# Performance work log

Measured on AMD Instinct MI355X. Metric: run time of the kernel, lower is better.

## Reference

```python
import jax, jax.numpy as jnp
import numpy as np

EPS = 1e-5
B, C, H, W, MIP, CQ = 2, 256, 64, 64, 8, 32  # MIP = max(8, C//32); CQ = C//8


def _bn(x, p):
    # inference BatchNorm; p is [4, C] = (gamma, beta, running_mean, running_var)
    g, b, m, v = p[0], p[1], p[2], p[3]
    s = g / jnp.sqrt(v + EPS)
    return x * s[None, :, None, None] + (b - m * s)[None, :, None, None]


def _c1(x, w):  # 1x1 conv, w: [O, I]
    return jnp.einsum('bchw,oc->bohw', x, w)


def _c3(x, w):  # 3x3 conv, SAME padding, w: [O, I, 3, 3]
    return jax.lax.conv_general_dilated(x, w, (1, 1), 'SAME',
                                        dimension_numbers=('NCHW', 'OIHW', 'NCHW'))


def _cbs1(x, w, p):  # Conv(1x1)+BN+SiLU (YOLOv7 Conv block)
    return jax.nn.silu(_bn(_c1(x, w), p))


def _cbs3(x, w, p):  # Conv(3x3)+BN+SiLU
    return jax.nn.silu(_bn(_c3(x, w), p))


def _maxpool(x, k):  # MaxPool2d(kernel=k, stride=1, padding=k//2)
    p = k // 2
    return jax.lax.reduce_window(x, -jnp.inf, jax.lax.max,
                                 (1, 1, k, k), (1, 1, 1, 1),
                                 ((0, 0), (0, 0), (p, p), (p, p)))


def setup_inputs() -> dict:
    ks = iter(jax.random.split(jax.random.key(0), 64))

    def rn(shape, scale):
        return jax.random.normal(next(ks), shape, jnp.float32) * scale

    def w_(o, i, k=1):  # fan-in scaled conv weight
        sc = 1.0 / float(np.sqrt(i * k * k))
        return rn((o, i) if k == 1 else (o, i, k, k), sc)

    def bnp(c):  # gamma, beta, running_mean, running_var (var > 0)
        return jnp.stack([1.0 + rn((c,), 0.05), rn((c,), 0.05), rn((c,), 0.05),
                          0.5 + jax.random.uniform(next(ks), (c,), jnp.float32)])

    cm = C  # SPPCSPC hidden: int(2*C*0.5) = C
    return dict(
        x=rn((B, C, H, W), 1.0),
        ca_w1=w_(MIP, C), ca_b1=rn((MIP,), 0.05), ca_bn=bnp(MIP),
        ca_wh=w_(C, MIP), ca_bh=rn((C,), 0.05),
        ca_ww=w_(C, MIP), ca_bw=rn((C,), 0.05),
        s1_w=w_(cm, C), s1_bn=bnp(cm),
        s2_w=w_(cm, C), s2_bn=bnp(cm),
        s3_w=w_(cm, cm, 3), s3_bn=bnp(cm),
        s4_w=w_(cm, cm), s4_bn=bnp(cm),
        s5_w=w_(cm, 4 * cm), s5_bn=bnp(cm),
        s6_w=w_(cm, cm, 3), s6_bn=bnp(cm),
        s7_w=w_(C, 2 * cm), s7_bn=bnp(C),
        pq_w=w_(CQ, C), pq_b=rn((CQ,), 0.05),
        pk_w=w_(CQ, C), pk_b=rn((CQ,), 0.05),
        pv_w=w_(C, C), pv_b=rn((C,), 0.05),
        gamma_pa=rn((1,), 1.0), gamma_ca=rn((1,), 1.0),
    )


def reference(x, ca_w1, ca_b1, ca_bn, ca_wh, ca_bh, ca_ww, ca_bw,
              s1_w, s1_bn, s2_w, s2_bn, s3_w, s3_bn, s4_w, s4_bn,
              s5_w, s5_bn, s6_w, s6_bn, s7_w, s7_bn,
              pq_w, pq_b, pk_w, pk_b, pv_w, pv_b, gamma_pa, gamma_ca):
    b, c, h, w = x.shape
    # ---- CoordAtt ----
    xh = jnp.mean(x, axis=3, keepdims=True)                                 # b,c,h,1
    xw = jnp.transpose(jnp.mean(x, axis=2, keepdims=True), (0, 1, 3, 2))    # b,c,w,1
    y = jnp.concatenate([xh, xw], axis=2)                                   # b,c,h+w,1
    y = _bn(_c1(y, ca_w1) + ca_b1[None, :, None, None], ca_bn)
    y = y * jnp.clip(y + 3.0, 0.0, 6.0) / 6.0                               # h_swish
    a_h = jax.nn.sigmoid(_c1(y[:, :, :h], ca_wh) + ca_bh[None, :, None, None])
    a_w = jax.nn.sigmoid(_c1(jnp.transpose(y[:, :, h:], (0, 1, 3, 2)), ca_ww)
                         + ca_bw[None, :, None, None])
    r = x * a_w * a_h
    # ---- SPPCSPC ----
    x1 = _cbs1(_cbs3(_cbs1(r, s1_w, s1_bn), s3_w, s3_bn), s4_w, s4_bn)
    cat = jnp.concatenate([x1] + [_maxpool(x1, k) for k in (5, 9, 13)], axis=1)
    y1 = _cbs3(_cbs1(cat, s5_w, s5_bn), s6_w, s6_bn)
    y2 = _cbs1(r, s2_w, s2_bn)
    res = _cbs1(jnp.concatenate([y1, y2], axis=1), s7_w, s7_bn)
    # ---- PAM (spatial attention) ----
    n = h * w
    f = res.reshape(b, c, n)
    q = jnp.einsum('bcn,oc->bon', f, pq_w) + pq_b[None, :, None]            # b,c/8,n
    k = jnp.einsum('bcn,oc->bon', f, pk_w) + pk_b[None, :, None]
    v = jnp.einsum('bcn,oc->bon', f, pv_w) + pv_b[None, :, None]            # b,c,n
    attn = jax.nn.softmax(jnp.einsum('bcn,bcm->bnm', q, k), axis=-1)        # b,n,n
    res_pa = gamma_pa * jnp.einsum('bcm,bnm->bcn', v, attn).reshape(b, c, h, w) + res
    # ---- CAM (channel attention) ----
    e = jnp.einsum('bcn,bdn->bcd', f, f)                                    # b,c,c
    attn_c = jax.nn.softmax(jnp.max(e, axis=-1, keepdims=True) - e, axis=-1)
    res_ca = gamma_ca * jnp.einsum('bcd,bdn->bcn', attn_c, f).reshape(b, c, h, w) + res
    return res + res_ca + res_pa
```

## Files before the change

### kernel.cpp

```cpp
#include <hip/hip_runtime.h>

typedef unsigned short u16;
typedef __attribute__((ext_vector_type(8))) short bf16x8;
typedef __attribute__((ext_vector_type(4))) float f32x4;
#define EPSV 1e-5f
#define LOG2E 1.4426950408889634f

__device__ __forceinline__ float b2f(u16 u) {
  union { float f; unsigned int i; } v; v.i = ((unsigned int)u) << 16; return v.f;
}
__device__ __forceinline__ u16 f2b(float f) {
  union { float f; unsigned int i; } v; v.f = f;
  unsigned int r = v.i + 0x7FFFu + ((v.i >> 16) & 1u);
  return (u16)(r >> 16);
}
__device__ __forceinline__ u16 f2b_trunc(float f) {
  union { float f; unsigned int i; } v; v.f = f;
  return (u16)(v.i >> 16);
}
__device__ __forceinline__ float silu_(float z) { return z / (1.f + exp2f(-LOG2E * z)); }

__global__ __launch_bounds__(128) void detect_k(const u16* __restrict__ xp, float* __restrict__ flag) {
  __shared__ int cnt[2];
  int t = threadIdx.x;
  if (t < 2) cnt[t] = 0;
  __syncthreads();
  u16 u = xp[t * 2];
  int e = (u >> 7) & 0xff;
  if (e != 0 && (e < 90 || e > 160)) atomicAdd(&cnt[0], 1);
  if (u == 0) atomicAdd(&cnt[1], 1);
  __syncthreads();
  if (t == 0) *flag = (cnt[0] > 16 || cnt[1] > 64) ? 1.f : 0.f;
}


struct ConvArgs {
  const void* src[30];
  long dst[30];
  int end[30];
  int mode[30];
};

__global__ __launch_bounds__(256) void convert_all(ConvArgs a, float* __restrict__ wsF,
                                                   u16* __restrict__ wsH,
                                                   const float* __restrict__ flagp, int total) {
  const int flag = (*flagp > 0.5f);
  int gid = blockIdx.x * 256 + threadIdx.x;
  if (gid >= total) return;
  #pragma unroll 1
  for (int s = 0; s < 30; ++s) {
    if (gid < a.end[s]) {
      int idx = gid - (s ? a.end[s - 1] : 0);
      if (a.mode[s] == 0) {
        float v = flag ? ((const float*)a.src[s])[idx] : b2f(((const u16*)a.src[s])[idx]);
        wsF[a.dst[s] + idx] = v;
      } else {
        u16 h = flag ? f2b(((const float*)a.src[s])[idx]) : ((const u16*)a.src[s])[idx];
        wsH[a.dst[s] + idx] = h;
      }
      return;
    }
  }
}

__global__ __launch_bounds__(256) void w3t(const float* __restrict__ Wsrc, u16* __restrict__ Wdst) {
  int idx = blockIdx.x * 256 + threadIdx.x;
  int ch = idx & 31;
  int o  = (idx >> 5) & 255;
  int tap = (idx >> 13) % 9;
  int c8 = (idx >> 13) / 9;
  int i = c8 * 32 + ch;
  Wdst[idx] = f2b(Wsrc[((long)o * 256 + i) * 9 + tap]);
}

__global__ __launch_bounds__(256) void cvtb(const float* __restrict__ src, u16* __restrict__ dst, int n8) {
  int i = blockIdx.x * 256 + threadIdx.x;
  if (i >= n8) return;
  float4 f0 = *(const float4*)(src + (long)i * 8);
  float4 f1 = *(const float4*)(src + (long)i * 8 + 4);
  union { u16 h[8]; uint4 q; } u;
  u.h[0]=f2b(f0.x); u.h[1]=f2b(f0.y); u.h[2]=f2b(f0.z); u.h[3]=f2b(f0.w);
  u.h[4]=f2b(f1.x); u.h[5]=f2b(f1.y); u.h[6]=f2b(f1.z); u.h[7]=f2b(f1.w);
  *(uint4*)(dst + (long)i * 8) = u.q;
}


__global__ __launch_bounds__(256) void plane_means(const float* __restrict__ x, float* __restrict__ yin) {
  __shared__ float pl[4096];
  int bc = blockIdx.x, t = threadIdx.x;
  const float* xp = x + (long)bc * 4096;
  for (int j = 0; j < 16; ++j) { int id = j * 256 + t; pl[id] = xp[id]; }
  __syncthreads();
  if (t < 64) {
    float s = 0.f;
    for (int w = 0; w < 64; ++w) s += pl[t * 64 + w];
    yin[(long)bc * 128 + t] = s * (1.f / 64.f);
  } else if (t < 128) {
    int w = t - 64; float s = 0.f;
    for (int h = 0; h < 64; ++h) s += pl[h * 64 + w];
    yin[(long)bc * 128 + 64 + w] = s * (1.f / 64.f);
  }
}

__global__ __launch_bounds__(128) void ca_conv1(const float* __restrict__ yin, const float* __restrict__ w1,
                                                const float* __restrict__ b1, const float* __restrict__ bnp,
                                                float* __restrict__ ybn) {
  int b = blockIdx.x, p = threadIdx.x;
  float acc[8] = {0.f,0.f,0.f,0.f,0.f,0.f,0.f,0.f};
  for (int c = 0; c < 256; ++c) {
    float yv = yin[((long)b * 256 + c) * 128 + p];
    #pragma unroll
    for (int o = 0; o < 8; ++o) acc[o] += w1[o * 256 + c] * yv;
  }
  #pragma unroll
  for (int o = 0; o < 8; ++o) {
    float z = acc[o] + b1[o];
    float g = bnp[o], bt = bnp[8 + o], mn = bnp[16 + o], vr = bnp[24 + o];
    float s = g * rsqrtf(vr + EPSV);
    z = z * s + (bt - mn * s);
    float hs = fminf(fmaxf(z + 3.f, 0.f), 6.f) * (1.f / 6.f);
    ybn[((long)b * 8 + o) * 128 + p] = z * hs;
  }
}

__global__ __launch_bounds__(128) void ca_gate(const float* __restrict__ ybn,
    const float* __restrict__ wh, const float* __restrict__ bh,
    const float* __restrict__ ww, const float* __restrict__ bw,
    float* __restrict__ ah, float* __restrict__ aw_) {
  int c = blockIdx.x, b = blockIdx.y, t = threadIdx.x;
  if (t < 64) {
    float d = 0.f;
    #pragma unroll
    for (int o = 0; o < 8; ++o) d += wh[c * 8 + o] * ybn[((long)b * 8 + o) * 128 + t];
    d += bh[c];
    ah[((long)b * 256 + c) * 64 + t] = 1.f / (1.f + exp2f(-LOG2E * d));
  } else {
    int w = t - 64;
    float d = 0.f;
    #pragma unroll
    for (int o = 0; o < 8; ++o) d += ww[c * 8 + o] * ybn[((long)b * 8 + o) * 128 + 64 + w];
    d += bw[c];
    aw_[((long)b * 256 + c) * 64 + w] = 1.f / (1.f + exp2f(-LOG2E * d));
  }
}

__global__ __launch_bounds__(256) void apply_ca(const float* __restrict__ x, const float* __restrict__ ah,
                                                const float* __restrict__ aw_, u16* __restrict__ r) {
  int idx = blockIdx.x * 256 + threadIdx.x;
  int n = idx & 4095, bc = idx >> 12;
  int h = n >> 6, w = n & 63;
  r[idx] = f2b(x[idx] * ah[bc * 64 + h] * aw_[bc * 64 + w]);
}


template<int ACT, int OUTH>
__global__ __launch_bounds__(256) void mfma_cbs(
    const u16* __restrict__ Wbf, long aBS,
    const u16* __restrict__ In, long bBS,
    void* __restrict__ Out, long oBS,
    int O, int K, int N,
    const float* __restrict__ bnp, const float* __restrict__ bias)
{
  __shared__ u16 As[64 * 40];
  __shared__ u16 Bs[64 * 40];
  __shared__ float albe[64][2];
  const int t = threadIdx.x;
  const int n0 = blockIdx.x * 64;
  const int o0 = blockIdx.y * 64;
  const int b  = blockIdx.z;
  const int w = t >> 6, l = t & 63, lq = l >> 4, lr = l & 15;
  const int wo = (w >> 1) * 32, wn = (w & 1) * 32;
  if (t < 64) {
    int o = o0 + t;
    float al = 1.f, be = 0.f;
    if (bnp) {
      float g = bnp[o], bt = bnp[O + o], mn = bnp[2 * O + o], vr = bnp[3 * O + o];
      al = g * rsqrtf(vr + EPSV); be = bt - mn * al;
    }
    if (bias) be += bias[o];
    albe[t][0] = al; albe[t][1] = be;
  }
  const u16* Ab = Wbf + (long)b * aBS;
  const u16* inb = In + (long)b * bBS + n0;
  const int ao = t >> 2, akq = (t & 3) * 8;
  const int bk = t >> 3, bn8 = (t & 7) * 8;
  f32x4 acc[2][2] = {};
  for (int kc = 0; kc < K; kc += 32) {
    __syncthreads();
    *(uint4*)&As[ao * 40 + akq] = *(const uint4*)(Ab + (long)(o0 + ao) * K + kc + akq);
    union { uint4 q; u16 h[8]; } tb;
    tb.q = *(const uint4*)(inb + (long)(kc + bk) * N + bn8);
    #pragma unroll
    for (int j = 0; j < 8; ++j) Bs[(bn8 + j) * 40 + bk] = tb.h[j];
    __syncthreads();
    bf16x8 af[2], bfv[2];
    #pragma unroll
    for (int i = 0; i < 2; ++i) af[i] = *(const bf16x8*)&As[(wo + i * 16 + lr) * 40 + lq * 8];
    #pragma unroll
    for (int j = 0; j < 2; ++j) bfv[j] = *(const bf16x8*)&Bs[(wn + j * 16 + lr) * 40 + lq * 8];
    #pragma unroll
    for (int i = 0; i < 2; ++i)
      #pragma unroll
      for (int j = 0; j < 2; ++j)
        acc[i][j] = __builtin_amdgcn_mfma_f32_16x16x32_bf16(af[i], bfv[j], acc[i][j], 0, 0, 0);
  }
  float* ob = (float*)Out + (long)b * oBS;
  u16* obh = (u16*)Out + (long)b * oBS;
  #pragma unroll
  for (int i = 0; i < 2; ++i) {
    #pragma unroll
    for (int r = 0; r < 4; ++r) {
      int ol = wo + i * 16 + lq * 4 + r;
      float al = albe[ol][0], be = albe[ol][1];
      #pragma unroll
      for (int j = 0; j < 2; ++j) {
        float vv = acc[i][j][r] * al + be;
        if (ACT) vv = silu_(vv);
        if (OUTH) obh[(long)(o0 + ol) * N + n0 + wn + j * 16 + lr] = f2b(vv);
        else      ob[(long)(o0 + ol) * N + n0 + wn + j * 16 + lr] = vv;
      }
    }
  }
}

__global__ __launch_bounds__(256) void conv3_mfma(
    const u16* __restrict__ Wt,
    const u16* __restrict__ In, long iBS,
    u16* __restrict__ Out, long oBS, int O, int I,
    const float* __restrict__ bnp)
{
  __shared__ u16 As[9 * 64 * 34];
  __shared__ u16 Bs[4 * 66 * 34];
  __shared__ float albe[64][2];
  const int t = threadIdx.x;
  const int h0 = blockIdx.x * 2;
  const int o0 = blockIdx.y * 64;
  const int b  = blockIdx.z;
  const int w = t >> 6, l = t & 63, lq = l >> 4, lr = l & 15;
  const int wo = (w >> 1) * 32, wn = (w & 1) * 64;
  if (t < 64) {
    int o = o0 + t;
    float g = bnp[o], bt = bnp[O + o], mn = bnp[2 * O + o], vr = bnp[3 * O + o];
    float al = g * rsqrtf(vr + EPSV);
    albe[t][0] = al; albe[t][1] = bt - mn * al;
  }
  {
    int r = t >> 6, cs = (t >> 5) & 1, ch = t & 31;
    Bs[(r * 66 + (cs ? 65 : 0)) * 34 + ch] = 0;
  }
  const u16* inb = In + (long)b * iBS;
  const int bch = t >> 3, bcg = (t & 7) * 8;
  f32x4 acc[2][4] = {};
  for (int c8 = 0; c8 < (I >> 5); ++c8) {
    __syncthreads();
    {
      const u16* wsrc = Wt + (long)c8 * 9 * 256 * 32;
      #pragma unroll
      for (int j = 0; j < 9; ++j) {
        int e = j * 2048 + t * 8;
        int tap = e >> 11, o = (e >> 5) & 63, ch0 = e & 31;
        uint4 vv = *(const uint4*)(wsrc + ((long)tap * 256 + o0 + o) * 32 + ch0);
        *(uint4*)&As[(tap * 64 + o) * 34 + ch0] = vv;
      }
    }
    {
      const u16* cbase = inb + (long)(c8 * 32 + bch) * 4096;
      #pragma unroll
      for (int r = 0; r < 4; ++r) {
        int row = h0 - 1 + r;
        union { uint4 q; u16 h[8]; } tb;
        if (row >= 0 && row < 64) {
          tb.q = *(const uint4*)(cbase + row * 64 + bcg);
        } else {
          tb.q = make_uint4(0, 0, 0, 0);
        }
        #pragma unroll
        for (int j2 = 0; j2 < 8; ++j2)
          Bs[(r * 66 + bcg + 1 + j2) * 34 + bch] = tb.h[j2];
      }
    }
    __syncthreads();
    #pragma unroll
    for (int dy = 0; dy < 3; ++dy) {
      #pragma unroll
      for (int dx = 0; dx < 3; ++dx) {
        const int tap = dy * 3 + dx;
        bf16x8 af0 = *(const bf16x8*)&As[(tap * 64 + wo + lr) * 34 + lq * 8];
        bf16x8 af1 = *(const bf16x8*)&As[(tap * 64 + wo + 16 + lr) * 34 + lq * 8];
        #pragma unroll
        for (int j = 0; j < 4; ++j) {
          int nb = wn + j * 16;
          int rowS = (nb >> 6) + dy;
          int colS = (nb & 63) + dx;
          bf16x8 bv = *(const bf16x8*)&Bs[(rowS * 66 + colS + lr) * 34 + lq * 8];
          acc[0][j] = __builtin_amdgcn_mfma_f32_16x16x32_bf16(af0, bv, acc[0][j], 0, 0, 0);
          acc[1][j] = __builtin_amdgcn_mfma_f32_16x16x32_bf16(af1, bv, acc[1][j], 0, 0, 0);
        }
      }
    }
  }
  u16* ob = Out + (long)b * oBS;
  const int n0 = h0 * 64;
  #pragma unroll
  for (int i = 0; i < 2; ++i) {
    #pragma unroll
    for (int r = 0; r < 4; ++r) {
      int ol = wo + i * 16 + lq * 4 + r;
      float al = albe[ol][0], be = albe[ol][1];
      #pragma unroll
      for (int j = 0; j < 4; ++j) {
        float vv = silu_(acc[i][j][r] * al + be);
        ob[(long)(o0 + ol) * 4096 + n0 + wn + j * 16 + lr] = f2b(vv);
      }
    }
  }
}

__global__ __launch_bounds__(256) void pool3(u16* __restrict__ cat, long bs) {
  __shared__ float A[68][72];
  __shared__ float Bb[68][72];
  const int t = threadIdx.x;
  const int c = blockIdx.x, b = blockIdx.y;
  u16* base = cat + (long)b * bs + (long)c * 4096;
  for (int i = t; i < 68 * 72; i += 256) { (&A[0][0])[i] = -1e30f; (&Bb[0][0])[i] = -1e30f; }
  __syncthreads();
  const int r = t >> 2, c0 = (t & 3) * 16;
  #pragma unroll
  for (int j = 0; j < 16; ++j) A[r + 2][c0 + 2 + j] = b2f(base[r * 64 + c0 + j]);
  const long CNu = 1048576;
  #pragma unroll 1
  for (int s = 1; s <= 3; ++s) {
    __syncthreads();
    #pragma unroll
    for (int j = 0; j < 16; ++j) {
      int cc = c0 + j;
      float m = fmaxf(fmaxf(fmaxf(A[r+2][cc], A[r+2][cc+1]), fmaxf(A[r+2][cc+2], A[r+2][cc+3])), A[r+2][cc+4]);
      Bb[r + 2][cc + 2] = m;
    }
    __syncthreads();
    u16* out = base + (long)s * CNu;
    #pragma unroll
    for (int j = 0; j < 16; ++j) {
      int hc = c0 + 2 + j;
      float m = fmaxf(fmaxf(fmaxf(Bb[r][hc], Bb[r+1][hc]), fmaxf(Bb[r+2][hc], Bb[r+3][hc])), Bb[r+4][hc]);
      out[r * 64 + c0 + j] = f2b_trunc(m);
      A[r + 2][hc] = m;
    }
  }
}

__global__ __launch_bounds__(256) void transpose_hh(const u16* __restrict__ in, u16* __restrict__ out) {
  __shared__ u16 tile[32][34];
  int b = blockIdx.z;
  int c0 = blockIdx.x * 32, r0 = blockIdx.y * 32;
  int tx = threadIdx.x & 31, ty = threadIdx.x >> 5;
  const u16* ib = in + (long)b * 262144;
  u16* ob = out + (long)b * 262144;
  #pragma unroll
  for (int i = 0; i < 4; ++i) {
    int r = r0 + ty + i * 8;
    tile[ty + i * 8][tx] = ib[(long)r * 4096 + c0 + tx];
  }
  __syncthreads();
  #pragma unroll
  for (int i = 0; i < 4; ++i) {
    int c = c0 + ty + i * 8;
    ob[(long)c * 64 + r0 + tx] = tile[tx][ty + i * 8];
  }
}

__global__ __launch_bounds__(256) void pam_qk_max(const u16* __restrict__ qkT, float* __restrict__ pmax) {
  __shared__ u16 Qs[32 * 40];
  __shared__ u16 Ks[64 * 40];
  __shared__ float red[4][32][17];
  const int t = threadIdx.x;
  const int b = blockIdx.z, ms = blockIdx.y, n0 = blockIdx.x * 32;
  const int w = t >> 6, l = t & 63, lq = l >> 4, lr = l & 15;
  const int wn = w & 1, wc = w >> 1;
  if (t < 128) {
    int row = t >> 2, cq = (t & 3) * 8;
    *(uint4*)&Qs[row * 40 + cq] = *(const uint4*)(qkT + ((long)b * 4096 + n0 + row) * 64 + cq);
  }
  __syncthreads();
  bf16x8 qf = *(const bf16x8*)&Qs[(wn * 16 + lr) * 40 + lq * 8];
  float mx4[4] = {-1e30f, -1e30f, -1e30f, -1e30f};
  const int krow = t >> 2, kcq = (t & 3) * 8;
  for (int it = 0; it < 16; ++it) {
    int m0 = ms * 1024 + it * 64;
    __syncthreads();
    *(uint4*)&Ks[krow * 40 + kcq] = *(const uint4*)(qkT + ((long)b * 4096 + m0 + krow) * 64 + 32 + kcq);
    __syncthreads();
    #pragma unroll
    for (int s = 0; s < 2; ++s) {
      int msub = wc * 2 + s;
      bf16x8 kf = *(const bf16x8*)&Ks[(msub * 16 + lr) * 40 + lq * 8];
      f32x4 S = {};
      S = __builtin_amdgcn_mfma_f32_16x16x32_bf16(qf, kf, S, 0, 0, 0);
      #pragma unroll
      for (int r = 0; r < 4; ++r) mx4[r] = fmaxf(mx4[r], S[r]);
    }
  }
  #pragma unroll
  for (int r = 0; r < 4; ++r) red[w][wn * 16 + lq * 4 + r][lr] = mx4[r];
  __syncthreads();
  if (t < 32) {
    int wbase = t >> 4;
    float M = -1e30f;
    #pragma unroll
    for (int j = 0; j < 2; ++j)
      #pragma unroll
      for (int l2 = 0; l2 < 16; ++l2)
        M = fmaxf(M, red[wbase + 2 * j][t][l2]);
    pmax[((long)ms * 2 + b) * 4096 + n0 + t] = M;
  }
}

__global__ __launch_bounds__(256) void pam_merge(const float* __restrict__ pmax, float* __restrict__ rmx) {
  int i = blockIdx.x * 256 + threadIdx.x;
  int b = i >> 12, n = i & 4095;
  float m = pmax[(long)b * 4096 + n];
  #pragma unroll
  for (int ms = 1; ms < 4; ++ms) m = fmaxf(m, pmax[((long)ms * 2 + b) * 4096 + n]);
  rmx[i] = m;
}

__global__ __launch_bounds__(512) void pam_attn(const u16* __restrict__ qkT,
    const u16* __restrict__ vb, const float* __restrict__ rowmax,
    float* __restrict__ Obase, float* __restrict__ Sbase) {
  __shared__ u16 Qs[32 * 40];
  __shared__ u16 Ks[64 * 40];
  __shared__ u16 Vs[256 * 72];
  __shared__ u16 Ps[32 * 72];
  __shared__ float rmL[32];
  __shared__ float srow[32];
  const int t = threadIdx.x;
  const int mh = blockIdx.y;
  const int b = blockIdx.z;
  const int n0 = blockIdx.x * 32;
  const int w = t >> 6, l = t & 63, lq = l >> 4, lr = l & 15;
  const int nf = w & 1;
  const int mf = w >> 1;
  const int cw = w * 32;
  float* O = Obase + (long)mh * 2097152;
  float* S = Sbase + (long)mh * 8192;
  if (t < 128) {
    int row = t >> 2, cq = (t & 3) * 8;
    *(uint4*)&Qs[row * 40 + cq] = *(const uint4*)(qkT + ((long)b * 4096 + n0 + row) * 64 + cq);
  }
  if (t < 32) { rmL[t] = rowmax[(long)b * 4096 + n0 + t] * LOG2E; srow[t] = 0.f; }
  __syncthreads();
  bf16x8 qf = *(const bf16x8*)&Qs[(nf * 16 + lr) * 40 + lq * 8];
  float rm4[4];
  #pragma unroll
  for (int r = 0; r < 4; ++r) rm4[r] = rmL[nf * 16 + lq * 4 + r];
  float sp[4] = {0.f, 0.f, 0.f, 0.f};
  f32x4 acc[2][2] = {};
  const int krow = t >> 3, kc4 = (t & 7) * 4;
  const int vcc = t >> 1, vm = (t & 1) * 32;
  const u16* kbase = qkT + ((long)b * 4096 + krow) * 64 + 32 + kc4;
  const u16* vbase = vb + ((long)b * 256 + vcc) * 4096 + vm;
  const int mStart = mh * 2048, mEnd = mStart + 2048;
  for (int m0 = mStart; m0 < mEnd; m0 += 64) {
    __syncthreads();
    *(uint2*)&Ks[krow * 40 + kc4] = *(const uint2*)(kbase + (long)m0 * 64);
    {
      const u16* src = vbase + m0;
      u16* dst = &Vs[vcc * 72 + vm];
      #pragma unroll
      for (int i = 0; i < 4; ++i) *(uint4*)(dst + i * 8) = *(const uint4*)(src + i * 8);
    }
    __syncthreads();
    {
      bf16x8 kf = *(const bf16x8*)&Ks[(mf * 16 + lr) * 40 + lq * 8];
      f32x4 Sv = {};
      Sv = __builtin_amdgcn_mfma_f32_16x16x32_bf16(qf, kf, Sv, 0, 0, 0);
      #pragma unroll
      for (int r = 0; r < 4; ++r) {
        float p = exp2f(Sv[r] * LOG2E - rm4[r]);
        sp[r] += p;
        Ps[(nf * 16 + lq * 4 + r) * 72 + mf * 16 + lr] = f2b_trunc(p);
      }
    }
    __syncthreads();
    #pragma unroll
    for (int ks = 0; ks < 2; ++ks) {
      bf16x8 pf0 = *(const bf16x8*)&Ps[lr * 72 + ks * 32 + lq * 8];
      bf16x8 pf1 = *(const bf16x8*)&Ps[(16 + lr) * 72 + ks * 32 + lq * 8];
      #pragma unroll
      for (int cf = 0; cf < 2; ++cf) {
        bf16x8 vf = *(const bf16x8*)&Vs[(cw + cf * 16 + lr) * 72 + ks * 32 + lq * 8];
        acc[cf][0] = __builtin_amdgcn_mfma_f32_16x16x32_bf16(vf, pf0, acc[cf][0], 0, 0, 0);
        acc[cf][1] = __builtin_amdgcn_mfma_f32_16x16x32_bf16(vf, pf1, acc[cf][1], 0, 0, 0);
      }
    }
  }
  #pragma unroll
  for (int r = 0; r < 4; ++r) {
    float s = sp[r];
    s += __shfl_xor(s, 1); s += __shfl_xor(s, 2);
    s += __shfl_xor(s, 4); s += __shfl_xor(s, 8);
    if (lr == 0) atomicAdd(&srow[nf * 16 + lq * 4 + r], s);
  }
  __syncthreads();
  if (t < 32) S[(long)b * 4096 + n0 + t] = srow[t];
  float* ob = O + (long)b * 1048576 + n0;
  #pragma unroll
  for (int cf = 0; cf < 2; ++cf) {
    #pragma unroll
    for (int r = 0; r < 4; ++r) {
      int c = cw + cf * 16 + lq * 4 + r;
      ob[(long)c * 4096 + lr]      = acc[cf][0][r];
      ob[(long)c * 4096 + 16 + lr] = acc[cf][1][r];
    }
  }
}


__global__ __launch_bounds__(256) void fillz(float* __restrict__ p, int n) {
  int i = blockIdx.x * 256 + threadIdx.x;
  if (i < n) p[i] = 0.f;
}

__global__ __launch_bounds__(256) void cam_e_mfma(const u16* __restrict__ resb, float* __restrict__ e) {
  __shared__ u16 As[64 * 40];
  __shared__ u16 Bs[128 * 40];
  const int t = threadIdx.x;
  const int d0 = blockIdx.x * 128;
  const int c0 = blockIdx.y * 64;
  const int bz = blockIdx.z;
  const int b = bz >> 4, ks = bz & 15;
  const int w = t >> 6, l = t & 63, lq = l >> 4, lr = l & 15;
  const int wo = (w >> 1) * 32, wn = (w & 1) * 64;
  const u16* fb = resb + (long)b * 1048576;
  const int ao = t >> 2, akq = (t & 3) * 8;
  const int bo = t >> 1, bkq = (t & 1) * 16;
  f32x4 acc[2][4] = {};
  for (int kc = ks * 256; kc < ks * 256 + 256; kc += 32) {
    __syncthreads();
    *(uint4*)&As[ao * 40 + akq] = *(const uint4*)(fb + (long)(c0 + ao) * 4096 + kc + akq);
    #pragma unroll
    for (int i = 0; i < 2; ++i)
      *(uint4*)&Bs[bo * 40 + bkq + i * 8] = *(const uint4*)(fb + (long)(d0 + bo) * 4096 + kc + bkq + i * 8);
    __syncthreads();
    bf16x8 af[2], bfv[4];
    #pragma unroll
    for (int i = 0; i < 2; ++i) af[i] = *(const bf16x8*)&As[(wo + i * 16 + lr) * 40 + lq * 8];
    #pragma unroll
    for (int j = 0; j < 4; ++j) bfv[j] = *(const bf16x8*)&Bs[(wn + j * 16 + lr) * 40 + lq * 8];
    #pragma unroll
    for (int i = 0; i < 2; ++i)
      #pragma unroll
      for (int j = 0; j < 4; ++j)
        acc[i][j] = __builtin_amdgcn_mfma_f32_16x16x32_bf16(af[i], bfv[j], acc[i][j], 0, 0, 0);
  }
  #pragma unroll
  for (int i = 0; i < 2; ++i)
    #pragma unroll
    for (int r = 0; r < 4; ++r) {
      int ol = wo + i * 16 + lq * 4 + r;
      #pragma unroll
      for (int j = 0; j < 4; ++j)
        atomicAdd(&e[((long)b << 16) + (long)(c0 + ol) * 256 + d0 + wn + j * 16 + lr], acc[i][j][r]);
    }
}

__global__ __launch_bounds__(256) void cam_softmax(const float* __restrict__ e, u16* __restrict__ attn) {
  __shared__ float red[256];
  int c = blockIdx.x, b = blockIdx.y, t = threadIdx.x;
  const float* row = e + ((long)b << 16) + (long)c * 256;
  float v = row[t];
  red[t] = v; __syncthreads();
  for (int s = 128; s > 0; s >>= 1) { if (t < s) red[t] = fminf(red[t], red[t + s]); __syncthreads(); }
  float emin = red[0]; __syncthreads();
  float ex = exp2f(LOG2E * (emin - v));
  red[t] = ex; __syncthreads();
  for (int s = 128; s > 0; s >>= 1) { if (t < s) red[t] += red[t + s]; __syncthreads(); }
  float inv = 1.f / red[0];
  attn[((long)b << 16) + (long)c * 256 + t] = f2b(ex * inv);
}


__global__ __launch_bounds__(256) void combine(const float* __restrict__ res, const float* __restrict__ O,
    const float* __restrict__ S, const float* __restrict__ cam, const float* __restrict__ gp,
    void* __restrict__ outp, const float* __restrict__ flagp) {
  int idx = blockIdx.x * 256 + threadIdx.x;
  int b = idx >> 20, n = idx & 4095;
  float g1 = gp[0], g2 = gp[1];
  float sden = S[(long)b * 4096 + n] + S[8192 + (long)b * 4096 + n];
  float pamv = (O[idx] + O[2097152 + idx]) / sden;
  float v = 3.f * res[idx] + g1 * pamv + g2 * cam[idx];
  if (*flagp > 0.5f) ((float*)outp)[idx] = v;
  else               ((u16*)outp)[idx] = f2b(v);
}


extern "C" void kernel_launch(void* const* d_in, const int* in_sizes, int n_in,
                              void* d_out, int out_size, void* d_ws, size_t ws_size,
                              hipStream_t stream)
{
  (void)out_size; (void)ws_size; (void)n_in;
  float* ws = (float*)d_ws;
  const long CN = 1048576;

  float* A  = ws;
  float* Bp = ws + 2 * CN;
  float* Cp = ws + 4 * CN;
  float* D  = ws + 6 * CN;
  const long WFo = 14 * CN;

  u16*   rB   = (u16*)A;
  float* res  = A;
  float* xf   = Bp;
  u16*   BpU  = (u16*)Bp;
  float* yin  = Cp;
  float* ybn  = Cp + 65536;
  float* ah   = Cp + 67584;
  float* aw_  = Cp + 100352;
  u16*   CpU  = (u16*)Cp;
  u16*   catU = (u16*)D;
  u16*   y12U = (u16*)D;
  float* D2   = D + 2 * CN;
  u16*   qkbU = (u16*)D2;
  u16*   qkTU = (u16*)(D2 + 262144);
  float* pmax = D2 + 524288;
  float* rmx  = D2 + 557056;
  float* e    = D2 + 565248;
  u16*   attnc= (u16*)(D2 + 696320);
  float* S0   = D2 + 761856;
  float* cam  = D;
  float* O0   = D + 4 * CN;

  ConvArgs ca;
  long fOff[30], hOff[30];
  long hcur = 0;
  float* flagp = ws + WFo;
  {
    long cum = 0, fcur = WFo + 4;
    for (int i = 0; i < 30; ++i) {
      ca.src[i] = d_in[i];
      int h = (i == 8 || i == 10 || i == 14 || i == 16 || i == 20 ||
               i == 22 || i == 24 || i == 26) ? 1 : 0;
      ca.mode[i] = h;
      if (i == 0) { ca.dst[i] = 2 * CN; fOff[i] = 2 * CN; }
      else if (h) { ca.dst[i] = hcur; hOff[i] = hcur; hcur += in_sizes[i]; }
      else        { ca.dst[i] = fcur; fOff[i] = fcur; fcur += in_sizes[i]; }
      cum += in_sizes[i];
      ca.end[i] = (int)cum;
    }
  }
  long fTotal = WFo + 4;
  for (int i = 1; i < 30; ++i) if (!ca.mode[i]) fTotal = (fOff[i] + in_sizes[i] > fTotal) ? fOff[i] + in_sizes[i] : fTotal;
  u16* wsH = (u16*)(ws + fTotal);
  u16* wt3a = wsH + hcur;
  u16* wt3b = wsH + hcur + 589824;
  int total = ca.end[29];

  detect_k<<<dim3(1), dim3(128), 0, stream>>>((const u16*)d_in[0], flagp);
  convert_all<<<dim3((total + 255) / 256), dim3(256), 0, stream>>>(ca, ws, wsH, flagp, total);

  float* ca_w1 = ws + fOff[1];
  float* ca_b1 = ws + fOff[2];
  float* ca_bn = ws + fOff[3];
  float* ca_wh = ws + fOff[4];
  float* ca_bh = ws + fOff[5];
  float* ca_ww = ws + fOff[6];
  float* ca_bw = ws + fOff[7];
  u16*   s1_w  = wsH + hOff[8];   float* s1_bn = ws + fOff[9];
  u16*   s2_w  = wsH + hOff[10];  float* s2_bn = ws + fOff[11];
  float* s3_wf = ws + fOff[12];   float* s3_bn = ws + fOff[13];
  u16*   s4_w  = wsH + hOff[14];  float* s4_bn = ws + fOff[15];
  u16*   s5_w  = wsH + hOff[16];  float* s5_bn = ws + fOff[17];
  float* s6_wf = ws + fOff[18];   float* s6_bn = ws + fOff[19];
  u16*   s7_w  = wsH + hOff[20];  float* s7_bn = ws + fOff[21];
  u16*   qk_w  = wsH + hOff[22];  float* qk_b  = ws + fOff[23];
  u16*   pv_w  = wsH + hOff[26];  float* pv_b  = ws + fOff[27];
  float* gammas = ws + fOff[28];

  w3t<<<dim3(2304), dim3(256), 0, stream>>>(s3_wf, wt3a);
  w3t<<<dim3(2304), dim3(256), 0, stream>>>(s6_wf, wt3b);

  plane_means<<<dim3(512), dim3(256), 0, stream>>>(xf, yin);
  ca_conv1<<<dim3(2), dim3(128), 0, stream>>>(yin, ca_w1, ca_b1, ca_bn, ybn);
  ca_gate<<<dim3(256, 2), dim3(128), 0, stream>>>(ybn, ca_wh, ca_bh, ca_ww, ca_bw, ah, aw_);
  apply_ca<<<dim3(8192), dim3(256), 0, stream>>>(xf, ah, aw_, rB);

  mfma_cbs<1,1><<<dim3(64, 4, 2), dim3(256), 0, stream>>>(s1_w, 0, rB, CN, CpU, CN, 256, 256, 4096, s1_bn, nullptr);
  conv3_mfma<<<dim3(32, 4, 2), dim3(256), 0, stream>>>(wt3a, CpU, CN, BpU, CN, 256, 256, s3_bn);
  mfma_cbs<1,1><<<dim3(64, 4, 2), dim3(256), 0, stream>>>(s4_w, 0, BpU, CN, catU, 4 * CN, 256, 256, 4096, s4_bn, nullptr);

  pool3<<<dim3(256, 2), dim3(256), 0, stream>>>(catU, 4 * CN);

  mfma_cbs<1,1><<<dim3(64, 4, 2), dim3(256), 0, stream>>>(s5_w, 0, catU, 4 * CN, BpU, CN, 256, 1024, 4096, s5_bn, nullptr);
  conv3_mfma<<<dim3(32, 4, 2), dim3(256), 0, stream>>>(wt3b, BpU, CN, y12U, 2 * CN, 256, 256, s6_bn);
  mfma_cbs<1,1><<<dim3(64, 4, 2), dim3(256), 0, stream>>>(s2_w, 0, rB, CN, y12U + CN, 2 * CN, 256, 256, 4096, s2_bn, nullptr);
  mfma_cbs<1,0><<<dim3(64, 4, 2), dim3(256), 0, stream>>>(s7_w, 0, y12U, 2 * CN, res, CN, 256, 512, 4096, s7_bn, nullptr);

  cvtb<<<dim3(1024), dim3(256), 0, stream>>>(res, BpU, 262144);
  mfma_cbs<0,1><<<dim3(64, 1, 2), dim3(256), 0, stream>>>(qk_w, 0, BpU, CN, qkbU, 262144, 64, 256, 4096, nullptr, qk_b);
  mfma_cbs<0,1><<<dim3(64, 4, 2), dim3(256), 0, stream>>>(pv_w, 0, BpU, CN, CpU, CN, 256, 256, 4096, nullptr, pv_b);
  transpose_hh<<<dim3(128, 2, 2), dim3(256), 0, stream>>>(qkbU, qkTU);

  pam_qk_max<<<dim3(128, 4, 2), dim3(256), 0, stream>>>(qkTU, pmax);
  pam_merge<<<dim3(32), dim3(256), 0, stream>>>(pmax, rmx);
  pam_attn<<<dim3(128, 2, 2), dim3(512), 0, stream>>>(qkTU, CpU, rmx, O0, S0);

  fillz<<<dim3(512), dim3(256), 0, stream>>>(e, 131072);
  cam_e_mfma<<<dim3(2, 4, 32), dim3(256), 0, stream>>>(BpU, e);
  cam_softmax<<<dim3(256, 2), dim3(256), 0, stream>>>(e, attnc);
  mfma_cbs<0,0><<<dim3(64, 4, 2), dim3(256), 0, stream>>>(attnc, 65536, BpU, CN, cam, CN, 256, 256, 4096, nullptr, nullptr);

  combine<<<dim3(8192), dim3(256), 0, stream>>>(res, O0, S0, cam, gammas, d_out, flagp);
}
```

Before: 457.4 us.

## Prefetch K/V tiles into registers and transpose score MFMA in PAM kernel

The PAM attention kernel now loads the next K and V tiles from global memory into registers while the current tile is being processed, so load latency overlaps with compute. The score MFMA operands are swapped, which transposes the accumulator layout. Each lane then holds four consecutive key positions for a single query row, allowing one packed 8-byte store into the P tile and a single row-max value per lane. The row-sum reduction shrinks to two shuffles, and s_setprio is raised around the PV MFMA block. The cost is higher register pressure from the prefetch buffers.

```diff
diff --git a/kernel.cpp b/kernel.cpp
--- a/kernel.cpp
+++ b/kernel.cpp
@@ -448,40 +448,52 @@
     *(uint4*)&Qs[row * 40 + cq] = *(const uint4*)(qkT + ((long)b * 4096 + n0 + row) * 64 + cq);
   }
   if (t < 32) { rmL[t] = rowmax[(long)b * 4096 + n0 + t] * LOG2E; srow[t] = 0.f; }
-  __syncthreads();
-  bf16x8 qf = *(const bf16x8*)&Qs[(nf * 16 + lr) * 40 + lq * 8];
-  float rm4[4];
-  #pragma unroll
-  for (int r = 0; r < 4; ++r) rm4[r] = rmL[nf * 16 + lq * 4 + r];
-  float sp[4] = {0.f, 0.f, 0.f, 0.f};
-  f32x4 acc[2][2] = {};
   const int krow = t >> 3, kc4 = (t & 7) * 4;
   const int vcc = t >> 1, vm = (t & 1) * 32;
   const u16* kbase = qkT + ((long)b * 4096 + krow) * 64 + 32 + kc4;
   const u16* vbase = vb + ((long)b * 256 + vcc) * 4096 + vm;
   const int mStart = mh * 2048, mEnd = mStart + 2048;
+
+  uint2 kreg = *(const uint2*)(kbase + (long)mStart * 64);
+  uint4 vreg[4];
+  #pragma unroll
+  for (int i = 0; i < 4; ++i) vreg[i] = *(const uint4*)(vbase + mStart + i * 8);
+
+  __syncthreads();
+  bf16x8 qf = *(const bf16x8*)&Qs[(nf * 16 + lr) * 40 + lq * 8];
+  const float rml = rmL[nf * 16 + lr];
+  float spl = 0.f;
+  f32x4 acc[2][2] = {};
+
   for (int m0 = mStart; m0 < mEnd; m0 += 64) {
     __syncthreads();
-    *(uint2*)&Ks[krow * 40 + kc4] = *(const uint2*)(kbase + (long)m0 * 64);
+    *(uint2*)&Ks[krow * 40 + kc4] = kreg;
     {
-      const u16* src = vbase + m0;
       u16* dst = &Vs[vcc * 72 + vm];
       #pragma unroll
-      for (int i = 0; i < 4; ++i) *(uint4*)(dst + i * 8) = *(const uint4*)(src + i * 8);
+      for (int i = 0; i < 4; ++i) *(uint4*)(dst + i * 8) = vreg[i];
+    }
+    if (m0 + 64 < mEnd) {
+      kreg = *(const uint2*)(kbase + (long)(m0 + 64) * 64);
+      #pragma unroll
+      for (int i = 0; i < 4; ++i) vreg[i] = *(const uint4*)(vbase + (m0 + 64) + i * 8);
     }
     __syncthreads();
     {
       bf16x8 kf = *(const bf16x8*)&Ks[(mf * 16 + lr) * 40 + lq * 8];
       f32x4 Sv = {};
-      Sv = __builtin_amdgcn_mfma_f32_16x16x32_bf16(qf, kf, Sv, 0, 0, 0);
+      Sv = __builtin_amdgcn_mfma_f32_16x16x32_bf16(kf, qf, Sv, 0, 0, 0);
+      union { u16 h[4]; uint2 q; } pk;
       #pragma unroll
       for (int r = 0; r < 4; ++r) {
-        float p = exp2f(Sv[r] * LOG2E - rm4[r]);
-        sp[r] += p;
-        Ps[(nf * 16 + lq * 4 + r) * 72 + mf * 16 + lr] = f2b_trunc(p);
+        float p = exp2f(Sv[r] * LOG2E - rml);
+        spl += p;
+        pk.h[r] = f2b_trunc(p);
       }
-    }
-    __syncthreads();
+      *(uint2*)&Ps[(nf * 16 + lr) * 72 + mf * 16 + lq * 4] = pk.q;
+    }
+    __syncthreads();
+    __builtin_amdgcn_s_setprio(1);
     #pragma unroll
     for (int ks = 0; ks < 2; ++ks) {
       bf16x8 pf0 = *(const bf16x8*)&Ps[lr * 72 + ks * 32 + lq * 8];
@@ -493,14 +505,11 @@
         acc[cf][1] = __builtin_amdgcn_mfma_f32_16x16x32_bf16(vf, pf1, acc[cf][1], 0, 0, 0);
       }
     }
-  }
-  #pragma unroll
-  for (int r = 0; r < 4; ++r) {
-    float s = sp[r];
-    s += __shfl_xor(s, 1); s += __shfl_xor(s, 2);
-    s += __shfl_xor(s, 4); s += __shfl_xor(s, 8);
-    if (lr == 0) atomicAdd(&srow[nf * 16 + lq * 4 + r], s);
-  }
+    __builtin_amdgcn_s_setprio(0);
+  }
+  spl += __shfl_xor(spl, 16);
+  spl += __shfl_xor(spl, 32);
+  if (l < 16) atomicAdd(&srow[nf * 16 + lr], spl);
   __syncthreads();
   if (t < 32) S[(long)b * 4096 + n0 + t] = srow[t];
   float* ob = O + (long)b * 1048576 + n0;
```

Measured after the change: 553.5 us. 21.0% more time.
